# Optimization experiments

Measured on AMD Instinct MI355X. Metric: run time of the kernel, lower is better.

Reference implementation:

```python
import jax, jax.numpy as jnp
import numpy as np

N = 50000
E = 800000
IN = 256
HID = 64
H12 = 4
LAT = 32
NEG_SLOPE = 0.2


def gat_conv(x, src, dst, W, a_src, a_dst, b, heads, out_ch, concat):
    """PyG GATConv (eval mode, add_self_loops already applied to src/dst).
    x: [N, F_in]; src/dst: [Etot]; W: [F_in, heads*out_ch]; a_*: [heads, out_ch]; b: bias.
    Returns (out, alpha[Etot, heads])."""
    n = x.shape[0]
    h = (x @ W).reshape(n, heads, out_ch)                 # [N,H,C]
    e_src = (h * a_src).sum(-1)                           # [N,H]
    e_dst = (h * a_dst).sum(-1)                           # [N,H]
    e = jax.nn.leaky_relu(e_src[src] + e_dst[dst], NEG_SLOPE)   # [Etot,H]
    emax = jax.ops.segment_max(e, dst, num_segments=n)
    ee = jnp.exp(e - emax[dst])
    denom = jax.ops.segment_sum(ee, dst, num_segments=n)
    alpha = ee / (denom[dst] + 1e-16)                     # segment softmax over incoming edges
    msg = h[src] * alpha[:, :, None]                      # [Etot,H,C]
    out = jax.ops.segment_sum(msg, dst, num_segments=n)   # [N,H,C]
    out = out.reshape(n, heads * out_ch) if concat else out.mean(axis=1)
    return out + b, alpha


def setup_inputs() -> dict:
    key = jax.random.key(0)
    ks = jax.random.split(key, 20)
    s = 0.1
    inp = {
        "x": jax.random.normal(ks[0], (N, IN), jnp.float32),
        "edge_index": jax.random.randint(ks[1], (2, E), 0, N, jnp.int32),
        "W1": jax.random.normal(ks[2], (IN, H12 * HID), jnp.float32) * s,
        "a1s": jax.random.normal(ks[3], (H12, HID), jnp.float32) * s,
        "a1d": jax.random.normal(ks[4], (H12, HID), jnp.float32) * s,
        "b1": jnp.zeros((H12 * HID,), jnp.float32),
        "W2": jax.random.normal(ks[5], (H12 * HID, H12 * HID), jnp.float32) * s,
        "a2s": jax.random.normal(ks[6], (H12, HID), jnp.float32) * s,
        "a2d": jax.random.normal(ks[7], (H12, HID), jnp.float32) * s,
        "b2": jnp.zeros((HID,), jnp.float32),
        "Wm": jax.random.normal(ks[8], (HID, LAT), jnp.float32) * s,
        "ams": jax.random.normal(ks[9], (1, LAT), jnp.float32) * s,
        "amd": jax.random.normal(ks[10], (1, LAT), jnp.float32) * s,
        "bm": jnp.zeros((LAT,), jnp.float32),
        # log_std head
        "Ws": jax.random.normal(ks[11], (HID, LAT), jnp.float32) * s,
        "ass": jax.random.normal(ks[12], (1, LAT), jnp.float32) * s,
        "asd": jax.random.normal(ks[13], (1, LAT), jnp.float32) * s,
        "bs": jnp.zeros((LAT,), jnp.float32),
    }
    return inp


def reference(x, edge_index, W1, a1s, a1d, b1, W2, a2s, a2d, b2,
              Wm, ams, amd, bm, Ws, ass, asd, bs):
    # GATConv adds self loops by default
    loops = jnp.arange(N, dtype=edge_index.dtype)
    src = jnp.concatenate([edge_index[0], loops])
    dst = jnp.concatenate([edge_index[1], loops])

    h1, a_w1 = gat_conv(x, src, dst, W1, a1s, a1d, b1, H12, HID, True)
    h1 = jax.nn.relu(h1)
    h2, a_w2 = gat_conv(h1, src, dst, W2, a2s, a2d, b2, H12, HID, False)
    h2 = jax.nn.relu(h2)  # dropout is identity in eval mode
    z_mean, a_wm = gat_conv(h2, src, dst, Wm, ams, amd, bm, 1, LAT, False)
    z_log_std, a_ws = gat_conv(h2, src, dst, Ws, ass, asd, bs, 1, LAT, False)
    return (z_mean, z_log_std, a_w1, a_w2, a_wm, a_ws)
```

## Files before the change

### kernel.cpp

```cpp
#include <hip/hip_runtime.h>
#include <cstdint>
#include <cstddef>

#define NN 50000
#define EE 800000
#define ETOT 850000
#define NEG_SLOPE 0.2f

typedef _Float16 f16;
typedef __attribute__((ext_vector_type(4))) _Float16 f16x4;
typedef __attribute__((ext_vector_type(8))) _Float16 f16x8;
typedef __attribute__((ext_vector_type(4))) float f32x4;


__global__ __launch_bounds__(256) void deg_kernel(const int* __restrict__ ei, int* __restrict__ deg) {
    int e = blockIdx.x * 256 + threadIdx.x;
    if (e >= ETOT) return;
    int d = (e < EE) ? ei[EE + e] : (e - EE);
    atomicAdd(&deg[d], 1);
}

__global__ __launch_bounds__(256) void scan1_kernel(const int* __restrict__ deg, int* __restrict__ offs,
                                                    int* __restrict__ bsum, int n) {
    __shared__ int sh[256];
    int i = blockIdx.x * 256 + threadIdx.x;
    int v = (i < n) ? deg[i] : 0;
    sh[threadIdx.x] = v;
    __syncthreads();
    for (int off = 1; off < 256; off <<= 1) {
        int t = (threadIdx.x >= off) ? sh[threadIdx.x - off] : 0;
        __syncthreads();
        sh[threadIdx.x] += t;
        __syncthreads();
    }
    if (i < n) offs[i] = sh[threadIdx.x] - v;
    if (threadIdx.x == 255) bsum[blockIdx.x] = sh[255];
}

__global__ __launch_bounds__(256) void scan2_kernel(int* __restrict__ bsum, int nb) {
    __shared__ int sh[256];
    int v = (threadIdx.x < nb) ? bsum[threadIdx.x] : 0;
    sh[threadIdx.x] = v;
    __syncthreads();
    for (int off = 1; off < 256; off <<= 1) {
        int t = (threadIdx.x >= off) ? sh[threadIdx.x - off] : 0;
        __syncthreads();
        sh[threadIdx.x] += t;
        __syncthreads();
    }
    if (threadIdx.x < nb) bsum[threadIdx.x] = sh[threadIdx.x] - v;
}

__global__ __launch_bounds__(256) void scan3_kernel(const int* __restrict__ bsum, int* __restrict__ offs,
                                                    int* __restrict__ cursor, int n) {
    int i = blockIdx.x * 256 + threadIdx.x;
    if (i < n) {
        int o = offs[i] + bsum[blockIdx.x];
        offs[i] = o;
        cursor[i] = o;
    }
}

__global__ __launch_bounds__(256) void fill_kernel(const int* __restrict__ ei, int* __restrict__ cursor,
                                                   int* __restrict__ csrc, int* __restrict__ ceid) {
    int e = blockIdx.x * 256 + threadIdx.x;
    if (e >= ETOT) return;
    int d, s;
    if (e < EE) { s = ei[e]; d = ei[EE + e]; } else { s = e - EE; d = e - EE; }
    int p = atomicAdd(&cursor[d], 1);
    csrc[p] = s;
    ceid[p] = e;
}


template<int K, bool AF32>
__global__ __launch_bounds__(256) void mfma_gemm(const void* __restrict__ Ap, const f16* __restrict__ Bt,
                                                 f16* __restrict__ C, int M, int N) {
    int w = threadIdx.x >> 6, lane = threadIdx.x & 63;
    int m0 = blockIdx.y * 128 + w * 32;
    int n0 = blockIdx.x * 64;
    int r = lane & 15, kb = lane >> 4;
    int ar0 = m0 + r;       if (ar0 > M - 1) ar0 = M - 1;
    int ar1 = m0 + 16 + r;  if (ar1 > M - 1) ar1 = M - 1;
    f32x4 acc[2][4] = {};
    const float* Af = (const float*)Ap;
    const f16*   Ah = (const f16*)Ap;
    size_t a0off = (size_t)ar0 * K + kb * 8;
    size_t a1off = (size_t)ar1 * K + kb * 8;
    const f16* bbase = Bt + (size_t)(n0 + r) * K + kb * 8;
    for (int k0 = 0; k0 < K; k0 += 32) {
        f16x8 a0, a1;
        if constexpr (AF32) {
            float4 l0 = *(const float4*)(Af + a0off + k0);
            float4 h0 = *(const float4*)(Af + a0off + k0 + 4);
            float4 l1 = *(const float4*)(Af + a1off + k0);
            float4 h1 = *(const float4*)(Af + a1off + k0 + 4);
            a0[0]=(f16)l0.x; a0[1]=(f16)l0.y; a0[2]=(f16)l0.z; a0[3]=(f16)l0.w;
            a0[4]=(f16)h0.x; a0[5]=(f16)h0.y; a0[6]=(f16)h0.z; a0[7]=(f16)h0.w;
            a1[0]=(f16)l1.x; a1[1]=(f16)l1.y; a1[2]=(f16)l1.z; a1[3]=(f16)l1.w;
            a1[4]=(f16)h1.x; a1[5]=(f16)h1.y; a1[6]=(f16)h1.z; a1[7]=(f16)h1.w;
        } else {
            a0 = *(const f16x8*)(Ah + a0off + k0);
            a1 = *(const f16x8*)(Ah + a1off + k0);
        }
#pragma unroll
        for (int ni = 0; ni < 4; ++ni) {
            f16x8 b = *(const f16x8*)(bbase + (size_t)ni * 16 * K + k0);
            acc[0][ni] = __builtin_amdgcn_mfma_f32_16x16x32_f16(a0, b, acc[0][ni], 0, 0, 0);
            acc[1][ni] = __builtin_amdgcn_mfma_f32_16x16x32_f16(a1, b, acc[1][ni], 0, 0, 0);
        }
    }
#pragma unroll
    for (int mi = 0; mi < 2; ++mi) {
#pragma unroll
        for (int i = 0; i < 4; ++i) {
            int row = m0 + mi * 16 + kb * 4 + i;
            if (row < M) {
#pragma unroll
                for (int ni = 0; ni < 4; ++ni)
                    C[(size_t)row * N + n0 + ni * 16 + r] = (f16)acc[mi][ni][i];
            }
        }
    }
}


__global__ __launch_bounds__(256) void packw_kernel(const float* __restrict__ W1, const float* __restrict__ W2,
                                                    const float* __restrict__ Wm, const float* __restrict__ Ws,
                                                    const float* __restrict__ ams, const float* __restrict__ ass,
                                                    const float* __restrict__ amd, const float* __restrict__ asd,
                                                    f16* __restrict__ Wt1, f16* __restrict__ Wt2,
                                                    f16* __restrict__ Wtms,
                                                    float* __restrict__ aS, float* __restrict__ aD) {
    int i = blockIdx.x * 256 + threadIdx.x;
    if (i < 65536) {
        int n = i >> 8, k = i & 255;
        Wt1[(size_t)n * 256 + k] = (f16)W1[(size_t)k * 256 + n];
        Wt2[(size_t)n * 256 + k] = (f16)W2[(size_t)k * 256 + n];
    }
    if (i < 4096) {
        int c = i >> 6, k = i & 63;
        float v = (c < 32) ? Wm[k * 32 + c] : Ws[k * 32 + (c - 32)];
        Wtms[(size_t)c * 64 + k] = (f16)v;
    }
    if (i < 64) {
        aS[i] = (i < 32) ? ams[i] : ass[i - 32];
        aD[i] = (i < 32) ? amd[i] : asd[i - 32];
    }
}


__global__ __launch_bounds__(256) void scores4_kernel(const f16* __restrict__ H, const float* __restrict__ aS,
                                                      const float* __restrict__ aD, float* __restrict__ es,
                                                      float* __restrict__ ed) {
    int wave = threadIdx.x >> 6, lane = threadIdx.x & 63;
    int n = blockIdx.x * 4 + wave;
    if (n >= NN) return;
    f16x4 h = *(const f16x4*)(H + (size_t)n * 256 + lane * 4);
    float4 s4 = *(const float4*)(aS + lane * 4);
    float4 d4 = *(const float4*)(aD + lane * 4);
    float hx = (float)h[0], hy = (float)h[1], hz = (float)h[2], hw = (float)h[3];
    float ps = hx * s4.x + hy * s4.y + hz * s4.z + hw * s4.w;
    float pd = hx * d4.x + hy * d4.y + hz * d4.z + hw * d4.w;
    for (int off = 1; off < 16; off <<= 1) { ps += __shfl_xor(ps, off); pd += __shfl_xor(pd, off); }
    if ((lane & 15) == 0) {
        int hh = lane >> 4;
        es[n * 4 + hh] = ps;
        ed[n * 4 + hh] = pd;
    }
}

__global__ __launch_bounds__(256) void scores_ms_kernel(const f16* __restrict__ H, const float* __restrict__ aS,
                                                        const float* __restrict__ aD, float* __restrict__ es,
                                                        float* __restrict__ ed) {
    int wave = threadIdx.x >> 6, lane = threadIdx.x & 63;
    int n = blockIdx.x * 4 + wave;
    if (n >= NN) return;
    float h = (float)H[(size_t)n * 64 + lane];
    float ps = h * aS[lane];
    float pd = h * aD[lane];
    for (int off = 1; off < 32; off <<= 1) { ps += __shfl_xor(ps, off); pd += __shfl_xor(pd, off); }
    if ((lane & 31) == 0) {
        int g = lane >> 5;
        es[n * 2 + g] = ps;
        ed[n * 2 + g] = pd;
    }
}

__device__ __forceinline__ float leaky(float v) { return v > 0.f ? v : NEG_SLOPE * v; }


__device__ __forceinline__ void softmax4(
    int n, int lane, const float* __restrict__ es, const float* __restrict__ ed,
    const int* __restrict__ offs, const int* __restrict__ csrc, const int* __restrict__ ceid,
    float* __restrict__ etmp, float* __restrict__ alpha_out, int start, int deg) {
    int h = lane >> 4, sub = lane & 15;
    float edh = ed[n * 4 + h];
    float m = -INFINITY;
    for (int j = sub; j < deg; j += 16) {
        int s = csrc[start + j];
        float v = leaky(es[s * 4 + h] + edh);
        etmp[(size_t)(start + j) * 4 + h] = v;
        m = fmaxf(m, v);
    }
    for (int off = 1; off < 16; off <<= 1) m = fmaxf(m, __shfl_xor(m, off));
    float dsum = 0.f;
    for (int j = sub; j < deg; j += 16) {
        float t = __expf(etmp[(size_t)(start + j) * 4 + h] - m);
        etmp[(size_t)(start + j) * 4 + h] = t;
        dsum += t;
    }
    for (int off = 1; off < 16; off <<= 1) dsum += __shfl_xor(dsum, off);
    float inv = 1.f / (dsum + 1e-16f);
    for (int j = sub; j < deg; j += 16) {
        float a = etmp[(size_t)(start + j) * 4 + h] * inv;
        etmp[(size_t)(start + j) * 4 + h] = a;
        alpha_out[(size_t)ceid[start + j] * 4 + h] = a;
    }
}

__global__ __launch_bounds__(256) void agg_concat_kernel(
    const f16* __restrict__ H, const float* __restrict__ es, const float* __restrict__ ed,
    const int* __restrict__ offs, const int* __restrict__ csrc, const int* __restrict__ ceid,
    const float* __restrict__ bias, f16* __restrict__ out, float* __restrict__ alpha_out,
    float* __restrict__ etmp) {
    int wave = threadIdx.x >> 6, lane = threadIdx.x & 63;
    int n = blockIdx.x * 4 + wave;
    if (n >= NN) return;
    int h = lane >> 4;
    int start = offs[n];
    int end = (n + 1 < NN) ? offs[n + 1] : ETOT;
    int deg = end - start;
    softmax4(n, lane, es, ed, offs, csrc, ceid, etmp, alpha_out, start, deg);
    int cbase = lane * 4;
    float4 acc0 = {}, acc1 = {}, acc2 = {}, acc3 = {};
    int j = 0;
    for (; j + 3 < deg; j += 4) {
        int p = start + j;
        int s0 = csrc[p], s1 = csrc[p + 1], s2 = csrc[p + 2], s3 = csrc[p + 3];
        float a0 = etmp[(size_t)p * 4 + h];
        float a1 = etmp[(size_t)(p + 1) * 4 + h];
        float a2 = etmp[(size_t)(p + 2) * 4 + h];
        float a3 = etmp[(size_t)(p + 3) * 4 + h];
        f16x4 v0 = *(const f16x4*)(H + (size_t)s0 * 256 + cbase);
        f16x4 v1 = *(const f16x4*)(H + (size_t)s1 * 256 + cbase);
        f16x4 v2 = *(const f16x4*)(H + (size_t)s2 * 256 + cbase);
        f16x4 v3 = *(const f16x4*)(H + (size_t)s3 * 256 + cbase);
        acc0.x += a0 * (float)v0[0]; acc0.y += a0 * (float)v0[1]; acc0.z += a0 * (float)v0[2]; acc0.w += a0 * (float)v0[3];
        acc1.x += a1 * (float)v1[0]; acc1.y += a1 * (float)v1[1]; acc1.z += a1 * (float)v1[2]; acc1.w += a1 * (float)v1[3];
        acc2.x += a2 * (float)v2[0]; acc2.y += a2 * (float)v2[1]; acc2.z += a2 * (float)v2[2]; acc2.w += a2 * (float)v2[3];
        acc3.x += a3 * (float)v3[0]; acc3.y += a3 * (float)v3[1]; acc3.z += a3 * (float)v3[2]; acc3.w += a3 * (float)v3[3];
    }
    for (; j < deg; ++j) {
        int p = start + j;
        int s0 = csrc[p];
        float a0 = etmp[(size_t)p * 4 + h];
        f16x4 v0 = *(const f16x4*)(H + (size_t)s0 * 256 + cbase);
        acc0.x += a0 * (float)v0[0]; acc0.y += a0 * (float)v0[1]; acc0.z += a0 * (float)v0[2]; acc0.w += a0 * (float)v0[3];
    }
    float4 acc;
    acc.x = (acc0.x + acc1.x) + (acc2.x + acc3.x);
    acc.y = (acc0.y + acc1.y) + (acc2.y + acc3.y);
    acc.z = (acc0.z + acc1.z) + (acc2.z + acc3.z);
    acc.w = (acc0.w + acc1.w) + (acc2.w + acc3.w);
    float4 b = *(const float4*)(bias + cbase);
    f16x4 r;
    r[0] = (f16)fmaxf(acc.x + b.x, 0.f);
    r[1] = (f16)fmaxf(acc.y + b.y, 0.f);
    r[2] = (f16)fmaxf(acc.z + b.z, 0.f);
    r[3] = (f16)fmaxf(acc.w + b.w, 0.f);
    *(f16x4*)(out + (size_t)n * 256 + cbase) = r;
}

__global__ __launch_bounds__(256) void agg_mean_kernel(
    const f16* __restrict__ H, const float* __restrict__ es, const float* __restrict__ ed,
    const int* __restrict__ offs, const int* __restrict__ csrc, const int* __restrict__ ceid,
    const float* __restrict__ bias, f16* __restrict__ out, float* __restrict__ alpha_out,
    float* __restrict__ etmp) {
    int wave = threadIdx.x >> 6, lane = threadIdx.x & 63;
    int n = blockIdx.x * 4 + wave;
    if (n >= NN) return;
    int h = lane >> 4;
    int start = offs[n];
    int end = (n + 1 < NN) ? offs[n + 1] : ETOT;
    int deg = end - start;
    softmax4(n, lane, es, ed, offs, csrc, ceid, etmp, alpha_out, start, deg);
    int cbase = lane * 4;
    float4 acc0 = {}, acc1 = {}, acc2 = {}, acc3 = {};
    int j = 0;
    for (; j + 3 < deg; j += 4) {
        int p = start + j;
        int s0 = csrc[p], s1 = csrc[p + 1], s2 = csrc[p + 2], s3 = csrc[p + 3];
        float a0 = etmp[(size_t)p * 4 + h];
        float a1 = etmp[(size_t)(p + 1) * 4 + h];
        float a2 = etmp[(size_t)(p + 2) * 4 + h];
        float a3 = etmp[(size_t)(p + 3) * 4 + h];
        f16x4 v0 = *(const f16x4*)(H + (size_t)s0 * 256 + cbase);
        f16x4 v1 = *(const f16x4*)(H + (size_t)s1 * 256 + cbase);
        f16x4 v2 = *(const f16x4*)(H + (size_t)s2 * 256 + cbase);
        f16x4 v3 = *(const f16x4*)(H + (size_t)s3 * 256 + cbase);
        acc0.x += a0 * (float)v0[0]; acc0.y += a0 * (float)v0[1]; acc0.z += a0 * (float)v0[2]; acc0.w += a0 * (float)v0[3];
        acc1.x += a1 * (float)v1[0]; acc1.y += a1 * (float)v1[1]; acc1.z += a1 * (float)v1[2]; acc1.w += a1 * (float)v1[3];
        acc2.x += a2 * (float)v2[0]; acc2.y += a2 * (float)v2[1]; acc2.z += a2 * (float)v2[2]; acc2.w += a2 * (float)v2[3];
        acc3.x += a3 * (float)v3[0]; acc3.y += a3 * (float)v3[1]; acc3.z += a3 * (float)v3[2]; acc3.w += a3 * (float)v3[3];
    }
    for (; j < deg; ++j) {
        int p = start + j;
        int s0 = csrc[p];
        float a0 = etmp[(size_t)p * 4 + h];
        f16x4 v0 = *(const f16x4*)(H + (size_t)s0 * 256 + cbase);
        acc0.x += a0 * (float)v0[0]; acc0.y += a0 * (float)v0[1]; acc0.z += a0 * (float)v0[2]; acc0.w += a0 * (float)v0[3];
    }
    float4 acc;
    acc.x = (acc0.x + acc1.x) + (acc2.x + acc3.x);
    acc.y = (acc0.y + acc1.y) + (acc2.y + acc3.y);
    acc.z = (acc0.z + acc1.z) + (acc2.z + acc3.z);
    acc.w = (acc0.w + acc1.w) + (acc2.w + acc3.w);
    acc.x += __shfl_xor(acc.x, 16); acc.y += __shfl_xor(acc.y, 16);
    acc.z += __shfl_xor(acc.z, 16); acc.w += __shfl_xor(acc.w, 16);
    acc.x += __shfl_xor(acc.x, 32); acc.y += __shfl_xor(acc.y, 32);
    acc.z += __shfl_xor(acc.z, 32); acc.w += __shfl_xor(acc.w, 32);
    if (lane < 16) {
        float4 b = *(const float4*)(bias + lane * 4);
        f16x4 r;
        r[0] = (f16)fmaxf(acc.x * 0.25f + b.x, 0.f);
        r[1] = (f16)fmaxf(acc.y * 0.25f + b.y, 0.f);
        r[2] = (f16)fmaxf(acc.z * 0.25f + b.z, 0.f);
        r[3] = (f16)fmaxf(acc.w * 0.25f + b.w, 0.f);
        *(f16x4*)(out + (size_t)n * 64 + lane * 4) = r;
    }
}

__global__ __launch_bounds__(256) void agg_ms_kernel(
    const f16* __restrict__ H, const float* __restrict__ es, const float* __restrict__ ed,
    const int* __restrict__ offs, const int* __restrict__ csrc, const int* __restrict__ ceid,
    const float* __restrict__ bm, const float* __restrict__ bs,
    float* __restrict__ zmean, float* __restrict__ zlog,
    float* __restrict__ a_wm, float* __restrict__ a_ws,
    float* __restrict__ etmp) {
    int wave = threadIdx.x >> 6, lane = threadIdx.x & 63;
    int n = blockIdx.x * 4 + wave;
    if (n >= NN) return;
    int g = lane >> 5, sub = lane & 31;
    int start = offs[n];
    int end = (n + 1 < NN) ? offs[n + 1] : ETOT;
    int deg = end - start;
    float edh = ed[n * 2 + g];
    float m = -INFINITY;
    for (int j = sub; j < deg; j += 32) {
        int s = csrc[start + j];
        float v = leaky(es[s * 2 + g] + edh);
        etmp[(size_t)(start + j) * 2 + g] = v;
        m = fmaxf(m, v);
    }
    for (int off = 1; off < 32; off <<= 1) m = fmaxf(m, __shfl_xor(m, off));
    float dsum = 0.f;
    for (int j = sub; j < deg; j += 32) {
        float t = __expf(etmp[(size_t)(start + j) * 2 + g] - m);
        etmp[(size_t)(start + j) * 2 + g] = t;
        dsum += t;
    }
    for (int off = 1; off < 32; off <<= 1) dsum += __shfl_xor(dsum, off);
    float inv = 1.f / (dsum + 1e-16f);
    for (int j = sub; j < deg; j += 32) {
        float a = etmp[(size_t)(start + j) * 2 + g] * inv;
        etmp[(size_t)(start + j) * 2 + g] = a;
        int eid = ceid[start + j];
        if (g == 0) a_wm[eid] = a; else a_ws[eid] = a;
    }
    float acc0 = 0.f, acc1 = 0.f, acc2 = 0.f, acc3 = 0.f;
    int j = 0;
    for (; j + 3 < deg; j += 4) {
        int p = start + j;
        int s0 = csrc[p], s1 = csrc[p + 1], s2 = csrc[p + 2], s3 = csrc[p + 3];
        float a0 = etmp[(size_t)p * 2 + g];
        float a1 = etmp[(size_t)(p + 1) * 2 + g];
        float a2 = etmp[(size_t)(p + 2) * 2 + g];
        float a3 = etmp[(size_t)(p + 3) * 2 + g];
        acc0 += a0 * (float)H[(size_t)s0 * 64 + lane];
        acc1 += a1 * (float)H[(size_t)s1 * 64 + lane];
        acc2 += a2 * (float)H[(size_t)s2 * 64 + lane];
        acc3 += a3 * (float)H[(size_t)s3 * 64 + lane];
    }
    for (; j < deg; ++j) {
        int p = start + j;
        int s0 = csrc[p];
        float a0 = etmp[(size_t)p * 2 + g];
        acc0 += a0 * (float)H[(size_t)s0 * 64 + lane];
    }
    float acc = (acc0 + acc1) + (acc2 + acc3);
    if (g == 0) zmean[(size_t)n * 32 + sub] = acc + bm[sub];
    else        zlog[(size_t)n * 32 + sub] = acc + bs[sub];
}


extern "C" void kernel_launch(void* const* d_in, const int* in_sizes, int n_in,
                              void* d_out, int out_size, void* d_ws, size_t ws_size,
                              hipStream_t stream) {
    const float* x   = (const float*)d_in[0];
    const int*   ei  = (const int*)d_in[1];
    const float* W1  = (const float*)d_in[2];
    const float* a1s = (const float*)d_in[3];
    const float* a1d = (const float*)d_in[4];
    const float* b1  = (const float*)d_in[5];
    const float* W2  = (const float*)d_in[6];
    const float* a2s = (const float*)d_in[7];
    const float* a2d = (const float*)d_in[8];
    const float* b2  = (const float*)d_in[9];
    const float* Wm  = (const float*)d_in[10];
    const float* ams = (const float*)d_in[11];
    const float* amd = (const float*)d_in[12];
    const float* bm  = (const float*)d_in[13];
    const float* Ws  = (const float*)d_in[14];
    const float* ass = (const float*)d_in[15];
    const float* asd = (const float*)d_in[16];
    const float* bs  = (const float*)d_in[17];

    float* out = (float*)d_out;
    float* zmean = out;
    float* zlog  = out + 1600000;
    float* a_w1  = out + 3200000;
    float* a_w2  = out + 6600000;
    float* a_wm  = out + 10000000;
    float* a_ws_o = out + 10850000;

    float* ws = (float*)d_ws;
    size_t o = 0;
    f16*   Hh   = (f16*)(ws + o); o += (size_t)NN * 128;
    f16*   h1h  = (f16*)(ws + o); o += (size_t)NN * 128;
    f16*   h2h  = (f16*)(ws + o); o += (size_t)NN * 32;
    float* etmp = ws + o; o += (size_t)ETOT * 4;
    float* es1  = ws + o; o += NN * 4;
    float* ed1  = ws + o; o += NN * 4;
    float* es2  = ws + o; o += NN * 4;
    float* ed2  = ws + o; o += NN * 4;
    float* esms = ws + o; o += NN * 2;
    float* edms = ws + o; o += NN * 2;
    f16*   Wt1  = (f16*)(ws + o); o += 32768;
    f16*   Wt2  = (f16*)(ws + o); o += 32768;
    f16*   Wtms = (f16*)(ws + o); o += 2048;
    float* aSms = ws + o; o += 64;
    float* aDms = ws + o; o += 64;
    int* deg    = (int*)(ws + o); o += NN;
    int* offs   = (int*)(ws + o); o += NN;
    int* cursor = (int*)(ws + o); o += NN;
    int* csrc   = (int*)(ws + o); o += ETOT;
    int* ceid   = (int*)(ws + o); o += ETOT;

    const int edgeBlocks = (ETOT + 255) / 256;
    const int nodeBlocks = (NN + 255) / 256;
    const int waveBlocks = (NN + 3) / 4;

    hipMemsetAsync(deg, 0, NN * sizeof(int), stream);
    deg_kernel<<<edgeBlocks, 256, 0, stream>>>(ei, deg);
    scan1_kernel<<<nodeBlocks, 256, 0, stream>>>(deg, offs, cursor , NN);
    scan2_kernel<<<1, 256, 0, stream>>>(cursor, nodeBlocks);
    scan3_kernel<<<nodeBlocks, 256, 0, stream>>>(cursor, offs, deg , NN);
    fill_kernel<<<edgeBlocks, 256, 0, stream>>>(ei, deg, csrc, ceid);

    packw_kernel<<<256, 256, 0, stream>>>(W1, W2, Wm, Ws, ams, ass, amd, asd, Wt1, Wt2, Wtms, aSms, aDms);

    dim3 gg1(4, (NN + 127) / 128);
    dim3 gg3(1, (NN + 127) / 128);
    mfma_gemm<256, true><<<gg1, 256, 0, stream>>>(x, Wt1, Hh, NN, 256);
    scores4_kernel<<<waveBlocks, 256, 0, stream>>>(Hh, a1s, a1d, es1, ed1);
    agg_concat_kernel<<<waveBlocks, 256, 0, stream>>>(Hh, es1, ed1, offs, csrc, ceid, b1, h1h, a_w1, etmp);

    mfma_gemm<256, false><<<gg1, 256, 0, stream>>>(h1h, Wt2, Hh, NN, 256);
    scores4_kernel<<<waveBlocks, 256, 0, stream>>>(Hh, a2s, a2d, es2, ed2);
    agg_mean_kernel<<<waveBlocks, 256, 0, stream>>>(Hh, es2, ed2, offs, csrc, ceid, b2, h2h, a_w2, etmp);

    mfma_gemm<64, false><<<gg3, 256, 0, stream>>>(h2h, Wtms, Hh, NN, 64);
    scores_ms_kernel<<<waveBlocks, 256, 0, stream>>>(Hh, aSms, aDms, esms, edms);
    agg_ms_kernel<<<waveBlocks, 256, 0, stream>>>(Hh, esms, edms, offs, csrc, ceid, bm, bs,
                                                  zmean, zlog, a_wm, a_ws_o, etmp);
}
```

Baseline: 569.6 us.

## Fuse softmax into aggregation, drop max pass and etmp buffer, widen gathers

Removes the per-edge scratch buffer and the max-subtraction pass. The softmax denominator is computed in one pass, then edge weights are recomputed inside the aggregation loop. Gathers use 8-wide f16 loads with each half-wave handling alternate edges, and partial sums are combined by shuffles. This saves global writes and reads of etmp and one pass over the edges. It adds redundant exp evaluations and drops max-stabilisation, which could overflow for large scores.

```diff
diff --git a/kernel.cpp b/kernel.cpp
--- a/kernel.cpp
+++ b/kernel.cpp
@@ -190,207 +190,211 @@
 __device__ __forceinline__ float leaky(float v) { return v > 0.f ? v : NEG_SLOPE * v; }
 
 
-__device__ __forceinline__ void softmax4(
-    int n, int lane, const float* __restrict__ es, const float* __restrict__ ed,
-    const int* __restrict__ offs, const int* __restrict__ csrc, const int* __restrict__ ceid,
-    float* __restrict__ etmp, float* __restrict__ alpha_out, int start, int deg) {
-    int h = lane >> 4, sub = lane & 15;
-    float edh = ed[n * 4 + h];
-    float m = -INFINITY;
-    for (int j = sub; j < deg; j += 16) {
-        int s = csrc[start + j];
-        float v = leaky(es[s * 4 + h] + edh);
-        etmp[(size_t)(start + j) * 4 + h] = v;
-        m = fmaxf(m, v);
-    }
-    for (int off = 1; off < 16; off <<= 1) m = fmaxf(m, __shfl_xor(m, off));
-    float dsum = 0.f;
-    for (int j = sub; j < deg; j += 16) {
-        float t = __expf(etmp[(size_t)(start + j) * 4 + h] - m);
-        etmp[(size_t)(start + j) * 4 + h] = t;
-        dsum += t;
-    }
-    for (int off = 1; off < 16; off <<= 1) dsum += __shfl_xor(dsum, off);
-    float inv = 1.f / (dsum + 1e-16f);
-    for (int j = sub; j < deg; j += 16) {
-        float a = etmp[(size_t)(start + j) * 4 + h] * inv;
-        etmp[(size_t)(start + j) * 4 + h] = a;
-        alpha_out[(size_t)ceid[start + j] * 4 + h] = a;
-    }
-}
-
 __global__ __launch_bounds__(256) void agg_concat_kernel(
     const f16* __restrict__ H, const float* __restrict__ es, const float* __restrict__ ed,
     const int* __restrict__ offs, const int* __restrict__ csrc, const int* __restrict__ ceid,
-    const float* __restrict__ bias, f16* __restrict__ out, float* __restrict__ alpha_out,
-    float* __restrict__ etmp) {
+    const float* __restrict__ bias, f16* __restrict__ out, float* __restrict__ alpha_out) {
     int wave = threadIdx.x >> 6, lane = threadIdx.x & 63;
     int n = blockIdx.x * 4 + wave;
     if (n >= NN) return;
-    int h = lane >> 4;
     int start = offs[n];
     int end = (n + 1 < NN) ? offs[n + 1] : ETOT;
     int deg = end - start;
-    softmax4(n, lane, es, ed, offs, csrc, ceid, etmp, alpha_out, start, deg);
-    int cbase = lane * 4;
-    float4 acc0 = {}, acc1 = {}, acc2 = {}, acc3 = {};
-    int j = 0;
-    for (; j + 3 < deg; j += 4) {
-        int p = start + j;
-        int s0 = csrc[p], s1 = csrc[p + 1], s2 = csrc[p + 2], s3 = csrc[p + 3];
-        float a0 = etmp[(size_t)p * 4 + h];
-        float a1 = etmp[(size_t)(p + 1) * 4 + h];
-        float a2 = etmp[(size_t)(p + 2) * 4 + h];
-        float a3 = etmp[(size_t)(p + 3) * 4 + h];
-        f16x4 v0 = *(const f16x4*)(H + (size_t)s0 * 256 + cbase);
-        f16x4 v1 = *(const f16x4*)(H + (size_t)s1 * 256 + cbase);
-        f16x4 v2 = *(const f16x4*)(H + (size_t)s2 * 256 + cbase);
-        f16x4 v3 = *(const f16x4*)(H + (size_t)s3 * 256 + cbase);
-        acc0.x += a0 * (float)v0[0]; acc0.y += a0 * (float)v0[1]; acc0.z += a0 * (float)v0[2]; acc0.w += a0 * (float)v0[3];
-        acc1.x += a1 * (float)v1[0]; acc1.y += a1 * (float)v1[1]; acc1.z += a1 * (float)v1[2]; acc1.w += a1 * (float)v1[3];
-        acc2.x += a2 * (float)v2[0]; acc2.y += a2 * (float)v2[1]; acc2.z += a2 * (float)v2[2]; acc2.w += a2 * (float)v2[3];
-        acc3.x += a3 * (float)v3[0]; acc3.y += a3 * (float)v3[1]; acc3.z += a3 * (float)v3[2]; acc3.w += a3 * (float)v3[3];
-    }
-    for (; j < deg; ++j) {
-        int p = start + j;
-        int s0 = csrc[p];
-        float a0 = etmp[(size_t)p * 4 + h];
-        f16x4 v0 = *(const f16x4*)(H + (size_t)s0 * 256 + cbase);
-        acc0.x += a0 * (float)v0[0]; acc0.y += a0 * (float)v0[1]; acc0.z += a0 * (float)v0[2]; acc0.w += a0 * (float)v0[3];
-    }
-    float4 acc;
-    acc.x = (acc0.x + acc1.x) + (acc2.x + acc3.x);
-    acc.y = (acc0.y + acc1.y) + (acc2.y + acc3.y);
-    acc.z = (acc0.z + acc1.z) + (acc2.z + acc3.z);
-    acc.w = (acc0.w + acc1.w) + (acc2.w + acc3.w);
-    float4 b = *(const float4*)(bias + cbase);
-    f16x4 r;
-    r[0] = (f16)fmaxf(acc.x + b.x, 0.f);
-    r[1] = (f16)fmaxf(acc.y + b.y, 0.f);
-    r[2] = (f16)fmaxf(acc.z + b.z, 0.f);
-    r[3] = (f16)fmaxf(acc.w + b.w, 0.f);
-    *(f16x4*)(out + (size_t)n * 256 + cbase) = r;
-}
+    int h16 = lane >> 4, sub = lane & 15;
+    float edh = ed[n * 4 + h16];
+    float dsum = 0.f;
+    for (int j = sub; j < deg; j += 16) {
+        int s = csrc[start + j];
+        dsum += __expf(leaky(es[s * 4 + h16] + edh));
+    }
+    for (int off = 1; off < 16; off <<= 1) dsum += __shfl_xor(dsum, off);
+    float inv = 1.f / (dsum + 1e-16f);
+    int half = lane >> 5;
+    int l5 = lane & 31;
+    int hh = l5 >> 3;
+    int c8 = l5 * 8;
+    float invh = __shfl(inv, hh << 4);
+    float edhh = __shfl(edh, hh << 4);
+    bool writer = ((l5 & 7) == 0);
+    float accv[8] = {};
+    int j = half;
+    for (; j + 6 < deg; j += 8) {
+        int p0 = start + j, p1 = start + j + 2, p2 = start + j + 4, p3 = start + j + 6;
+        int s0 = csrc[p0], s1 = csrc[p1], s2 = csrc[p2], s3 = csrc[p3];
+        float a0 = __expf(leaky(es[s0 * 4 + hh] + edhh)) * invh;
+        float a1 = __expf(leaky(es[s1 * 4 + hh] + edhh)) * invh;
+        float a2 = __expf(leaky(es[s2 * 4 + hh] + edhh)) * invh;
+        float a3 = __expf(leaky(es[s3 * 4 + hh] + edhh)) * invh;
+        if (writer) {
+            alpha_out[(size_t)ceid[p0] * 4 + hh] = a0;
+            alpha_out[(size_t)ceid[p1] * 4 + hh] = a1;
+            alpha_out[(size_t)ceid[p2] * 4 + hh] = a2;
+            alpha_out[(size_t)ceid[p3] * 4 + hh] = a3;
+        }
+        f16x8 v0 = *(const f16x8*)(H + (size_t)s0 * 256 + c8);
+        f16x8 v1 = *(const f16x8*)(H + (size_t)s1 * 256 + c8);
+        f16x8 v2 = *(const f16x8*)(H + (size_t)s2 * 256 + c8);
+        f16x8 v3 = *(const f16x8*)(H + (size_t)s3 * 256 + c8);
+#pragma unroll
+        for (int k = 0; k < 8; ++k)
+            accv[k] += a0 * (float)v0[k] + a1 * (float)v1[k] + a2 * (float)v2[k] + a3 * (float)v3[k];
+    }
+    for (; j < deg; j += 2) {
+        int p0 = start + j;
+        int s0 = csrc[p0];
+        float a0 = __expf(leaky(es[s0 * 4 + hh] + edhh)) * invh;
+        if (writer) alpha_out[(size_t)ceid[p0] * 4 + hh] = a0;
+        f16x8 v0 = *(const f16x8*)(H + (size_t)s0 * 256 + c8);
+#pragma unroll
+        for (int k = 0; k < 8; ++k) accv[k] += a0 * (float)v0[k];
+    }
+#pragma unroll
+    for (int k = 0; k < 8; ++k) accv[k] += __shfl_xor(accv[k], 32);
+    if (lane < 32) {
+        f16x8 r;
+#pragma unroll
+        for (int k = 0; k < 8; ++k) r[k] = (f16)fmaxf(accv[k] + bias[c8 + k], 0.f);
+        *(f16x8*)(out + (size_t)n * 256 + c8) = r;
+    }
+}
+
 
 __global__ __launch_bounds__(256) void agg_mean_kernel(
     const f16* __restrict__ H, const float* __restrict__ es, const float* __restrict__ ed,
     const int* __restrict__ offs, const int* __restrict__ csrc, const int* __restrict__ ceid,
-    const float* __restrict__ bias, f16* __restrict__ out, float* __restrict__ alpha_out,
-    float* __restrict__ etmp) {
+    const float* __restrict__ bias, f16* __restrict__ out, float* __restrict__ alpha_out) {
     int wave = threadIdx.x >> 6, lane = threadIdx.x & 63;
     int n = blockIdx.x * 4 + wave;
     if (n >= NN) return;
-    int h = lane >> 4;
     int start = offs[n];
     int end = (n + 1 < NN) ? offs[n + 1] : ETOT;
     int deg = end - start;
-    softmax4(n, lane, es, ed, offs, csrc, ceid, etmp, alpha_out, start, deg);
-    int cbase = lane * 4;
-    float4 acc0 = {}, acc1 = {}, acc2 = {}, acc3 = {};
-    int j = 0;
-    for (; j + 3 < deg; j += 4) {
-        int p = start + j;
-        int s0 = csrc[p], s1 = csrc[p + 1], s2 = csrc[p + 2], s3 = csrc[p + 3];
-        float a0 = etmp[(size_t)p * 4 + h];
-        float a1 = etmp[(size_t)(p + 1) * 4 + h];
-        float a2 = etmp[(size_t)(p + 2) * 4 + h];
-        float a3 = etmp[(size_t)(p + 3) * 4 + h];
-        f16x4 v0 = *(const f16x4*)(H + (size_t)s0 * 256 + cbase);
-        f16x4 v1 = *(const f16x4*)(H + (size_t)s1 * 256 + cbase);
-        f16x4 v2 = *(const f16x4*)(H + (size_t)s2 * 256 + cbase);
-        f16x4 v3 = *(const f16x4*)(H + (size_t)s3 * 256 + cbase);
-        acc0.x += a0 * (float)v0[0]; acc0.y += a0 * (float)v0[1]; acc0.z += a0 * (float)v0[2]; acc0.w += a0 * (float)v0[3];
-        acc1.x += a1 * (float)v1[0]; acc1.y += a1 * (float)v1[1]; acc1.z += a1 * (float)v1[2]; acc1.w += a1 * (float)v1[3];
-        acc2.x += a2 * (float)v2[0]; acc2.y += a2 * (float)v2[1]; acc2.z += a2 * (float)v2[2]; acc2.w += a2 * (float)v2[3];
-        acc3.x += a3 * (float)v3[0]; acc3.y += a3 * (float)v3[1]; acc3.z += a3 * (float)v3[2]; acc3.w += a3 * (float)v3[3];
-    }
-    for (; j < deg; ++j) {
-        int p = start + j;
-        int s0 = csrc[p];
-        float a0 = etmp[(size_t)p * 4 + h];
-        f16x4 v0 = *(const f16x4*)(H + (size_t)s0 * 256 + cbase);
-        acc0.x += a0 * (float)v0[0]; acc0.y += a0 * (float)v0[1]; acc0.z += a0 * (float)v0[2]; acc0.w += a0 * (float)v0[3];
-    }
-    float4 acc;
-    acc.x = (acc0.x + acc1.x) + (acc2.x + acc3.x);
-    acc.y = (acc0.y + acc1.y) + (acc2.y + acc3.y);
-    acc.z = (acc0.z + acc1.z) + (acc2.z + acc3.z);
-    acc.w = (acc0.w + acc1.w) + (acc2.w + acc3.w);
-    acc.x += __shfl_xor(acc.x, 16); acc.y += __shfl_xor(acc.y, 16);
-    acc.z += __shfl_xor(acc.z, 16); acc.w += __shfl_xor(acc.w, 16);
-    acc.x += __shfl_xor(acc.x, 32); acc.y += __shfl_xor(acc.y, 32);
-    acc.z += __shfl_xor(acc.z, 32); acc.w += __shfl_xor(acc.w, 32);
-    if (lane < 16) {
-        float4 b = *(const float4*)(bias + lane * 4);
-        f16x4 r;
-        r[0] = (f16)fmaxf(acc.x * 0.25f + b.x, 0.f);
-        r[1] = (f16)fmaxf(acc.y * 0.25f + b.y, 0.f);
-        r[2] = (f16)fmaxf(acc.z * 0.25f + b.z, 0.f);
-        r[3] = (f16)fmaxf(acc.w * 0.25f + b.w, 0.f);
-        *(f16x4*)(out + (size_t)n * 64 + lane * 4) = r;
-    }
-}
+    int h16 = lane >> 4, sub = lane & 15;
+    float edh = ed[n * 4 + h16];
+    float dsum = 0.f;
+    for (int j = sub; j < deg; j += 16) {
+        int s = csrc[start + j];
+        dsum += __expf(leaky(es[s * 4 + h16] + edh));
+    }
+    for (int off = 1; off < 16; off <<= 1) dsum += __shfl_xor(dsum, off);
+    float inv = 1.f / (dsum + 1e-16f);
+    int half = lane >> 5;
+    int l5 = lane & 31;
+    int hh = l5 >> 3;
+    int c8 = l5 * 8;
+    float invh = __shfl(inv, hh << 4);
+    float edhh = __shfl(edh, hh << 4);
+    bool writer = ((l5 & 7) == 0);
+    float accv[8] = {};
+    int j = half;
+    for (; j + 6 < deg; j += 8) {
+        int p0 = start + j, p1 = start + j + 2, p2 = start + j + 4, p3 = start + j + 6;
+        int s0 = csrc[p0], s1 = csrc[p1], s2 = csrc[p2], s3 = csrc[p3];
+        float a0 = __expf(leaky(es[s0 * 4 + hh] + edhh)) * invh;
+        float a1 = __expf(leaky(es[s1 * 4 + hh] + edhh)) * invh;
+        float a2 = __expf(leaky(es[s2 * 4 + hh] + edhh)) * invh;
+        float a3 = __expf(leaky(es[s3 * 4 + hh] + edhh)) * invh;
+        if (writer) {
+            alpha_out[(size_t)ceid[p0] * 4 + hh] = a0;
+            alpha_out[(size_t)ceid[p1] * 4 + hh] = a1;
+            alpha_out[(size_t)ceid[p2] * 4 + hh] = a2;
+            alpha_out[(size_t)ceid[p3] * 4 + hh] = a3;
+        }
+        f16x8 v0 = *(const f16x8*)(H + (size_t)s0 * 256 + c8);
+        f16x8 v1 = *(const f16x8*)(H + (size_t)s1 * 256 + c8);
+        f16x8 v2 = *(const f16x8*)(H + (size_t)s2 * 256 + c8);
+        f16x8 v3 = *(const f16x8*)(H + (size_t)s3 * 256 + c8);
+#pragma unroll
+        for (int k = 0; k < 8; ++k)
+            accv[k] += a0 * (float)v0[k] + a1 * (float)v1[k] + a2 * (float)v2[k] + a3 * (float)v3[k];
+    }
+    for (; j < deg; j += 2) {
+        int p0 = start + j;
+        int s0 = csrc[p0];
+        float a0 = __expf(leaky(es[s0 * 4 + hh] + edhh)) * invh;
+        if (writer) alpha_out[(size_t)ceid[p0] * 4 + hh] = a0;
+        f16x8 v0 = *(const f16x8*)(H + (size_t)s0 * 256 + c8);
+#pragma unroll
+        for (int k = 0; k < 8; ++k) accv[k] += a0 * (float)v0[k];
+    }
+#pragma unroll
+    for (int k = 0; k < 8; ++k) {
+        accv[k] += __shfl_xor(accv[k], 8);
+        accv[k] += __shfl_xor(accv[k], 16);
+        accv[k] += __shfl_xor(accv[k], 32);
+    }
+    if (lane < 8) {
+        f16x8 r;
+#pragma unroll
+        for (int k = 0; k < 8; ++k) r[k] = (f16)fmaxf(accv[k] * 0.25f + bias[lane * 8 + k], 0.f);
+        *(f16x8*)(out + (size_t)n * 64 + lane * 8) = r;
+    }
+}
+
 
 __global__ __launch_bounds__(256) void agg_ms_kernel(
     const f16* __restrict__ H, const float* __restrict__ es, const float* __restrict__ ed,
     const int* __restrict__ offs, const int* __restrict__ csrc, const int* __restrict__ ceid,
     const float* __restrict__ bm, const float* __restrict__ bs,
     float* __restrict__ zmean, float* __restrict__ zlog,
-    float* __restrict__ a_wm, float* __restrict__ a_ws,
-    float* __restrict__ etmp) {
+    float* __restrict__ a_wm, float* __restrict__ a_ws) {
     int wave = threadIdx.x >> 6, lane = threadIdx.x & 63;
     int n = blockIdx.x * 4 + wave;
     if (n >= NN) return;
-    int g = lane >> 5, sub = lane & 31;
     int start = offs[n];
     int end = (n + 1 < NN) ? offs[n + 1] : ETOT;
     int deg = end - start;
-    float edh = ed[n * 2 + g];
-    float m = -INFINITY;
+    int g = lane >> 5, sub = lane & 31;
+    float edg = ed[n * 2 + g];
+    float dsum = 0.f;
     for (int j = sub; j < deg; j += 32) {
         int s = csrc[start + j];
-        float v = leaky(es[s * 2 + g] + edh);
-        etmp[(size_t)(start + j) * 2 + g] = v;
-        m = fmaxf(m, v);
-    }
-    for (int off = 1; off < 32; off <<= 1) m = fmaxf(m, __shfl_xor(m, off));
-    float dsum = 0.f;
-    for (int j = sub; j < deg; j += 32) {
-        float t = __expf(etmp[(size_t)(start + j) * 2 + g] - m);
-        etmp[(size_t)(start + j) * 2 + g] = t;
-        dsum += t;
+        dsum += __expf(leaky(es[s * 2 + g] + edg));
     }
     for (int off = 1; off < 32; off <<= 1) dsum += __shfl_xor(dsum, off);
     float inv = 1.f / (dsum + 1e-16f);
-    for (int j = sub; j < deg; j += 32) {
-        float a = etmp[(size_t)(start + j) * 2 + g] * inv;
-        etmp[(size_t)(start + j) * 2 + g] = a;
-        int eid = ceid[start + j];
-        if (g == 0) a_wm[eid] = a; else a_ws[eid] = a;
-    }
-    float acc0 = 0.f, acc1 = 0.f, acc2 = 0.f, acc3 = 0.f;
-    int j = 0;
-    for (; j + 3 < deg; j += 4) {
+    int slot = lane >> 3;
+    int le = lane & 7;
+    int g2 = le >> 2;
+    int c8 = le * 8;
+    float invg = __shfl(inv, g2 << 5);
+    float edg2 = __shfl(edg, g2 << 5);
+    float accv[8] = {};
+    for (int j = slot; j < deg; j += 8) {
         int p = start + j;
-        int s0 = csrc[p], s1 = csrc[p + 1], s2 = csrc[p + 2], s3 = csrc[p + 3];
-        float a0 = etmp[(size_t)p * 2 + g];
-        float a1 = etmp[(size_t)(p + 1) * 2 + g];
-        float a2 = etmp[(size_t)(p + 2) * 2 + g];
-        float a3 = etmp[(size_t)(p + 3) * 2 + g];
-        acc0 += a0 * (float)H[(size_t)s0 * 64 + lane];
-        acc1 += a1 * (float)H[(size_t)s1 * 64 + lane];
-        acc2 += a2 * (float)H[(size_t)s2 * 64 + lane];
-        acc3 += a3 * (float)H[(size_t)s3 * 64 + lane];
-    }
-    for (; j < deg; ++j) {
-        int p = start + j;
-        int s0 = csrc[p];
-        float a0 = etmp[(size_t)p * 2 + g];
-        acc0 += a0 * (float)H[(size_t)s0 * 64 + lane];
-    }
-    float acc = (acc0 + acc1) + (acc2 + acc3);
-    if (g == 0) zmean[(size_t)n * 32 + sub] = acc + bm[sub];
-    else        zlog[(size_t)n * 32 + sub] = acc + bs[sub];
+        int s = csrc[p];
+        float a = __expf(leaky(es[s * 2 + g2] + edg2)) * invg;
+        if (le == 0) a_wm[ceid[p]] = a;
+        else if (le == 4) a_ws[ceid[p]] = a;
+        f16x8 v = *(const f16x8*)(H + (size_t)s * 64 + c8);
+#pragma unroll
+        for (int k = 0; k < 8; ++k) accv[k] += a * (float)v[k];
+    }
+#pragma unroll
+    for (int k = 0; k < 8; ++k) {
+        accv[k] += __shfl_xor(accv[k], 8);
+        accv[k] += __shfl_xor(accv[k], 16);
+        accv[k] += __shfl_xor(accv[k], 32);
+    }
+    if (lane < 4) {
+        float4 r0, r1;
+        int cb = lane * 8;
+        r0.x = accv[0] + bm[cb + 0]; r0.y = accv[1] + bm[cb + 1];
+        r0.z = accv[2] + bm[cb + 2]; r0.w = accv[3] + bm[cb + 3];
+        r1.x = accv[4] + bm[cb + 4]; r1.y = accv[5] + bm[cb + 5];
+        r1.z = accv[6] + bm[cb + 6]; r1.w = accv[7] + bm[cb + 7];
+        *(float4*)(zmean + (size_t)n * 32 + cb) = r0;
+        *(float4*)(zmean + (size_t)n * 32 + cb + 4) = r1;
+    } else if (lane < 8) {
+        float4 r0, r1;
+        int cb = (lane - 4) * 8;
+        r0.x = accv[0] + bs[cb + 0]; r0.y = accv[1] + bs[cb + 1];
+        r0.z = accv[2] + bs[cb + 2]; r0.w = accv[3] + bs[cb + 3];
+        r1.x = accv[4] + bs[cb + 4]; r1.y = accv[5] + bs[cb + 5];
+        r1.z = accv[6] + bs[cb + 6]; r1.w = accv[7] + bs[cb + 7];
+        *(float4*)(zlog + (size_t)n * 32 + cb) = r0;
+        *(float4*)(zlog + (size_t)n * 32 + cb + 4) = r1;
+    }
 }
 
 
@@ -429,7 +433,6 @@
     f16*   Hh   = (f16*)(ws + o); o += (size_t)NN * 128;
     f16*   h1h  = (f16*)(ws + o); o += (size_t)NN * 128;
     f16*   h2h  = (f16*)(ws + o); o += (size_t)NN * 32;
-    float* etmp = ws + o; o += (size_t)ETOT * 4;
     float* es1  = ws + o; o += NN * 4;
     float* ed1  = ws + o; o += NN * 4;
     float* es2  = ws + o; o += NN * 4;
@@ -464,14 +467,14 @@
     dim3 gg3(1, (NN + 127) / 128);
     mfma_gemm<256, true><<<gg1, 256, 0, stream>>>(x, Wt1, Hh, NN, 256);
     scores4_kernel<<<waveBlocks, 256, 0, stream>>>(Hh, a1s, a1d, es1, ed1);
-    agg_concat_kernel<<<waveBlocks, 256, 0, stream>>>(Hh, es1, ed1, offs, csrc, ceid, b1, h1h, a_w1, etmp);
+    agg_concat_kernel<<<waveBlocks, 256, 0, stream>>>(Hh, es1, ed1, offs, csrc, ceid, b1, h1h, a_w1);
 
     mfma_gemm<256, false><<<gg1, 256, 0, stream>>>(h1h, Wt2, Hh, NN, 256);
     scores4_kernel<<<waveBlocks, 256, 0, stream>>>(Hh, a2s, a2d, es2, ed2);
-    agg_mean_kernel<<<waveBlocks, 256, 0, stream>>>(Hh, es2, ed2, offs, csrc, ceid, b2, h2h, a_w2, etmp);
+    agg_mean_kernel<<<waveBlocks, 256, 0, stream>>>(Hh, es2, ed2, offs, csrc, ceid, b2, h2h, a_w2);
 
     mfma_gemm<64, false><<<gg3, 256, 0, stream>>>(h2h, Wtms, Hh, NN, 64);
     scores_ms_kernel<<<waveBlocks, 256, 0, stream>>>(Hh, aSms, aDms, esms, edms);
     agg_ms_kernel<<<waveBlocks, 256, 0, stream>>>(Hh, esms, edms, offs, csrc, ceid, bm, bs,
-                                                  zmean, zlog, a_wm, a_ws_o, etmp);
-}
+                                                  zmean, zlog, a_wm, a_ws_o);
+}
```

Result: faster. 546.6 us (-4.0%).
